# Optimization experiments

Measured on AMD Instinct MI355X. Metric: run time of the kernel, lower is better.

The kernel has to match this reference:

```python
import jax, jax.numpy as jnp
import numpy as np

B, S, D, H, DFF = 2, 4096, 512, 8, 2048
DK = D // H
EPS = 1e-6


def layer_norm(x, alpha, bias):
    # torch: (x - mean) / (std + eps), std unbiased (ddof=1), eps added to std
    mean = jnp.mean(x, axis=-1, keepdims=True)
    std = jnp.std(x, axis=-1, keepdims=True, ddof=1)
    return alpha * (x - mean) / (std + EPS) + bias


def setup_inputs() -> dict:
    key = jax.random.key(0)
    ks = jax.random.split(key, 10)
    s = 0.02
    return {
        "x": jax.random.normal(ks[0], (B, S, D), jnp.float32),
        "mask": jax.random.randint(ks[1], (S, S), 0, 2, jnp.int32),
        "w_q": jax.random.normal(ks[2], (D, D), jnp.float32) * s,
        "w_k": jax.random.normal(ks[3], (D, D), jnp.float32) * s,
        "w_v": jax.random.normal(ks[4], (D, D), jnp.float32) * s,
        "w_o": jax.random.normal(ks[5], (D, D), jnp.float32) * s,
        "w1": jax.random.normal(ks[6], (D, DFF), jnp.float32) * s,
        "b1": jnp.zeros((DFF,), jnp.float32),
        "w2": jax.random.normal(ks[7], (DFF, D), jnp.float32) * s,
        "b2": jnp.zeros((D,), jnp.float32),
        "ln1_a": jnp.ones((D,), jnp.float32),
        "ln1_b": jnp.zeros((D,), jnp.float32),
        "ln2_a": jnp.ones((D,), jnp.float32),
        "ln2_b": jnp.zeros((D,), jnp.float32),
    }


def reference(x, mask, w_q, w_k, w_v, w_o, w1, b1, w2, b2, ln1_a, ln1_b, ln2_a, ln2_b):
    # --- sublayer 0: pre-norm self-attention with residual (dropout=0/eval) ---
    h = layer_norm(x, ln1_a, ln1_b)                       # [B,S,D]
    q = (h @ w_q).reshape(B, S, H, DK)
    k = (h @ w_k).reshape(B, S, H, DK)
    v = (h @ w_v).reshape(B, S, H, DK)
    scores = jnp.einsum("bqhd,bkhd->bhqk", q, k) / jnp.sqrt(jnp.float32(DK))
    scores = jnp.where(mask[None, None, :, :] == 0, jnp.float32(-1e9), scores)
    attn = jax.nn.softmax(scores, axis=-1)                # [B,H,S,S]
    ctx = jnp.einsum("bhqk,bkhd->bqhd", attn, v).reshape(B, S, D)
    x = x + ctx @ w_o
    # --- sublayer 1: pre-norm FFN with residual ---
    h2 = layer_norm(x, ln2_a, ln2_b)
    ff = jax.nn.relu(h2 @ w1 + b1) @ w2 + b2
    return x + ff
```

## Files before the change

### kernel.cpp

```cpp
#include <hip/hip_runtime.h>
#include <hip/hip_bf16.h>
#include <stdint.h>

#define S_LEN 4096
#define DMODEL 512
#define NHEAD 8
#define DHEAD 64
#define NTOK 8192

typedef unsigned short ushort_t;
typedef __attribute__((ext_vector_type(8))) short short8;
typedef __attribute__((ext_vector_type(4))) float f32x4;
typedef unsigned long long u64;
typedef __attribute__((ext_vector_type(2))) unsigned uint2v;

__device__ __forceinline__ float bf2f(ushort_t h) {
    union { unsigned u; float f; } c; c.u = ((unsigned)h) << 16; return c.f;
}
__device__ __forceinline__ ushort_t f2bf(float f) {
    union { float f; unsigned u; } c; c.f = f;
    unsigned u = c.u + 0x7fffu + ((c.u >> 16) & 1u);
    return (ushort_t)(u >> 16);
}
__device__ __forceinline__ void glds16(const ushort_t* g, ushort_t* l) {
    __builtin_amdgcn_global_load_lds(
        (const __attribute__((address_space(1))) unsigned int*)g,
        (__attribute__((address_space(3))) unsigned int*)l, 16, 0, 0);
}

__global__ __launch_bounds__(256) void maskbits_kernel(const int* __restrict__ mask,
        u64* __restrict__ mb) {
    size_t id = (size_t)blockIdx.x * 256 + threadIdx.x;
    int v = mask[id];
    u64 bits = __ballot(v != 0);
    if ((threadIdx.x & 63) == 0) mb[id >> 6] = bits;
}

__global__ __launch_bounds__(256) void wtrans_all(const float* __restrict__ wq,
        const float* __restrict__ wk, const float* __restrict__ wv,
        const float* __restrict__ wo, const float* __restrict__ w1,
        const float* __restrict__ w2,
        ushort_t* wqT, ushort_t* wkT, ushort_t* wvT, ushort_t* woT,
        ushort_t* w1T, ushort_t* w2T) {
    __shared__ __attribute__((aligned(16))) ushort_t t[64][72];
    int z = blockIdx.z;
    const float* src; ushort_t* dst; int R, C;
    switch (z) {
        case 0: src = wq; dst = wqT; R = 512;  C = 512;  break;
        case 1: src = wk; dst = wkT; R = 512;  C = 512;  break;
        case 2: src = wv; dst = wvT; R = 512;  C = 512;  break;
        case 3: src = wo; dst = woT; R = 512;  C = 512;  break;
        case 4: src = w1; dst = w1T; R = 512;  C = 2048; break;
        default: src = w2; dst = w2T; R = 2048; C = 512; break;
    }
    int r0 = blockIdx.x * 64, c0 = blockIdx.y * 64;
    if (r0 >= R || c0 >= C) return;
    int tid = threadIdx.x;
    for (int i = tid; i < 4096; i += 256) {
        int r = i >> 6, c = i & 63;
        t[r][c] = f2bf(src[(size_t)(r0 + r) * C + c0 + c]);
    }
    __syncthreads();
    for (int i = tid; i < 512; i += 256) {
        int c = i >> 3, rb = i & 7;
        short8 vv;
#pragma unroll
        for (int j = 0; j < 8; j++) ((ushort_t*)&vv)[j] = t[rb * 8 + j][c];
        *(short8*)(dst + (size_t)(c0 + c) * R + r0 + rb * 8) = vv;
    }
}

__global__ __launch_bounds__(256) void ln_f32(const float* __restrict__ x,
        const float* __restrict__ ga, const float* __restrict__ be,
        ushort_t* __restrict__ out) {
    int tok = blockIdx.x * 4 + (threadIdx.x >> 6);
    int lane = threadIdx.x & 63;
    const float* xr = x + (size_t)tok * DMODEL + lane * 8;
    f32x4 v0 = *(const f32x4*)xr;
    f32x4 v1 = *(const f32x4*)(xr + 4);
    float f[8];
    float s = 0.f, s2 = 0.f;
#pragma unroll
    for (int i = 0; i < 8; i++) {
        f[i] = (i < 4) ? v0[i] : v1[i - 4];
        s += f[i]; s2 += f[i] * f[i];
    }
#pragma unroll
    for (int off = 1; off < 64; off <<= 1) {
        s += __shfl_xor(s, off);
        s2 += __shfl_xor(s2, off);
    }
    float mean = s * (1.f / DMODEL);
    float var = (s2 - (float)DMODEL * mean * mean) * (1.f / (DMODEL - 1));
    var = fmaxf(var, 0.f);
    float inv = 1.f / (sqrtf(var) + 1e-6f);
    short8 o;
#pragma unroll
    for (int i = 0; i < 8; i++) {
        float val = ga[lane * 8 + i] * (f[i] - mean) * inv + be[lane * 8 + i];
        ((ushort_t*)&o)[i] = f2bf(val);
    }
    *(short8*)(out + (size_t)tok * DMODEL + lane * 8) = o;
}

__global__ __launch_bounds__(256) void vtrans(const ushort_t* __restrict__ V,
        ushort_t* __restrict__ VT) {
    __shared__ __attribute__((aligned(16))) ushort_t t[64][72];
    int s0 = blockIdx.x * 64;
    int bh = blockIdx.y;
    int b = bh >> 3, h = bh & 7;
    int tid = threadIdx.x;
    const ushort_t* src = V + ((size_t)b * S_LEN + s0) * DMODEL + h * DHEAD;
    for (int i = tid; i < 512; i += 256) {
        int r = i >> 3, cb = i & 7;
        *(short8*)&t[r][cb * 8] = *(const short8*)(src + (size_t)r * DMODEL + cb * 8);
    }
    __syncthreads();
    ushort_t* dst = VT + (size_t)bh * DHEAD * S_LEN;
    for (int i = tid; i < 512; i += 256) {
        int d = i >> 3, rb = i & 7;
        short8 vv;
#pragma unroll
        for (int j = 0; j < 8; j++) ((ushort_t*)&vv)[j] = t[rb * 8 + j][d];
        *(short8*)(dst + (size_t)d * S_LEN + s0 + rb * 8) = vv;
    }
}

template <int MW, int NW>
__device__ __forceinline__ void gemm_body(const ushort_t* __restrict__ A,
        const ushort_t* __restrict__ BT, void* __restrict__ C,
        int N, int K, float scale, const float* __restrict__ bias,
        const float* __restrict__ res, int relu, int cf32,
        ushort_t* As, ushort_t* Bs, int m0, int n0, int aoff, int coff) {
    int tid = threadIdx.x;
    int wave = tid >> 6, lane = tid & 63;
    int wm = wave >> 1, wn = wave & 1;
    int lr = lane & 15, lg = lane >> 4;
    int srow = lane >> 2, spos = lane & 3;
    int swz = (spos ^ ((srow >> 1) & 3)) * 8;
    int rdw = (lr >> 1) & 3;
    f32x4 acc[MW][NW];
#pragma unroll
    for (int i = 0; i < MW; i++)
#pragma unroll
        for (int j = 0; j < NW; j++) acc[i][j] = (f32x4){0.f, 0.f, 0.f, 0.f};

    const ushort_t* Ag = A + (size_t)(m0 - aoff) * K;
    const ushort_t* Bg = BT + (size_t)n0 * K;

    for (int k0 = 0; k0 < K; k0 += 32) {
        __syncthreads();
        for (int ia = wave; ia < 2 * MW; ia += 4)
            glds16(Ag + (size_t)(ia * 16 + srow) * K + k0 + swz, As + ia * 16 * 32);
        for (int ib = wave; ib < 2 * NW; ib += 4)
            glds16(Bg + (size_t)(ib * 16 + srow) * K + k0 + swz, Bs + ib * 16 * 32);
        __syncthreads();
        short8 af[MW], bfv[NW];
#pragma unroll
        for (int t = 0; t < MW; t++)
            af[t] = *(const short8*)(As + (wm * 16 * MW + t * 16 + lr) * 32 + (lg ^ rdw) * 8);
#pragma unroll
        for (int t = 0; t < NW; t++)
            bfv[t] = *(const short8*)(Bs + (wn * 16 * NW + t * 16 + lr) * 32 + (lg ^ rdw) * 8);
#pragma unroll
        for (int i = 0; i < MW; i++)
#pragma unroll
            for (int j = 0; j < NW; j++)
                acc[i][j] = __builtin_amdgcn_mfma_f32_16x16x32_bf16(af[i], bfv[j], acc[i][j], 0, 0, 0);
    }
#pragma unroll
    for (int i = 0; i < MW; i++) {
        int row = m0 + wm * 16 * MW + i * 16 + lg * 4;
#pragma unroll
        for (int j = 0; j < NW; j++) {
            int col = n0 + wn * 16 * NW + j * 16 + lr;
            float bb = bias ? bias[col] : 0.f;
#pragma unroll
            for (int r = 0; r < 4; r++) {
                float v = acc[i][j][r] * scale + bb;
                if (relu) v = fmaxf(v, 0.f);
                if (res) v += res[(size_t)(row + r) * N + col];
                size_t cidx = (size_t)(row + r - coff) * N + col;
                if (cf32) ((float*)C)[cidx] = v;
                else      ((ushort_t*)C)[cidx] = f2bf(v);
            }
        }
    }
}

__global__ __launch_bounds__(256) void gemm_bt128(const ushort_t* __restrict__ A,
        const ushort_t* __restrict__ BT, void* __restrict__ C,
        int N, int K, float scale, const float* bias, const float* res, int relu,
        int cf32, int m_base, int aoff, int coff) {
    __shared__ __attribute__((aligned(16))) ushort_t As[128 * 32];
    __shared__ __attribute__((aligned(16))) ushort_t Bs[128 * 32];
    gemm_body<4, 4>(A, BT, C, N, K, scale, bias, res, relu, cf32, As, Bs,
                    m_base + blockIdx.x * 128, blockIdx.y * 128, aoff, coff);
}

__global__ __launch_bounds__(256) void gemm_bt128x64(const ushort_t* __restrict__ A,
        const ushort_t* __restrict__ BT, void* __restrict__ C,
        int N, int K, float scale, const float* bias, const float* res, int relu,
        int cf32, int m_base, int aoff, int coff) {
    __shared__ __attribute__((aligned(16))) ushort_t As[128 * 32];
    __shared__ __attribute__((aligned(16))) ushort_t Bs[64 * 32];
    gemm_body<4, 2>(A, BT, C, N, K, scale, bias, res, relu, cf32, As, Bs,
                    m_base + blockIdx.x * 128, blockIdx.y * 64, aoff, coff);
}

__global__ __launch_bounds__(256) void gemm_qkv(const ushort_t* __restrict__ A,
        const ushort_t* __restrict__ wqT, const ushort_t* __restrict__ wkT,
        const ushort_t* __restrict__ wvT,
        ushort_t* __restrict__ Q, ushort_t* __restrict__ Kb, ushort_t* __restrict__ V) {
    __shared__ __attribute__((aligned(16))) ushort_t As[128 * 32];
    __shared__ __attribute__((aligned(16))) ushort_t Bs[128 * 32];
    int z = blockIdx.z;
    const ushort_t* W = (z == 0) ? wqT : ((z == 1) ? wkT : wvT);
    ushort_t* O = (z == 0) ? Q : ((z == 1) ? Kb : V);
    float sc = (z == 0) ? 0.18033688011112042f : 1.f;
    gemm_body<4, 4>(A, W, O, DMODEL, DMODEL, sc, nullptr, nullptr, 0, 0, As, Bs,
                    blockIdx.x * 128, blockIdx.y * 128, 0, 0);
}

__global__ __launch_bounds__(128, 4) void attn_kernel(const ushort_t* __restrict__ Q,
        const ushort_t* __restrict__ K, const ushort_t* __restrict__ VT,
        const unsigned* __restrict__ mb32, ushort_t* __restrict__ Opart,
        float* __restrict__ lpart) {
    __shared__ __attribute__((aligned(16))) ushort_t Ks[2][32 * 64];
    __shared__ __attribute__((aligned(16))) ushort_t Vs[2][64 * 32];
    int qt = blockIdx.x, h = blockIdx.y, zz = blockIdx.z;
    int b = zz >> 1, half = zz & 1;
    int tid = threadIdx.x;
    int wv = __builtin_amdgcn_readfirstlane(tid >> 6);
    int lane = tid & 63;
    int lr = lane & 15, lg = lane >> 4;
    size_t tokbase = (size_t)b * S_LEN;
    int q0 = qt * 64 + wv * 32;
    int k0 = half * (S_LEN / 2);

    const ushort_t* Qp = Q + (tokbase + q0) * DMODEL + h * DHEAD;
    short8 qf[2][2];
#pragma unroll
    for (int u = 0; u < 2; u++) {
        qf[u][0] = *(const short8*)(Qp + (size_t)(u * 16 + lr) * DMODEL + lg * 8);
        qf[u][1] = *(const short8*)(Qp + (size_t)(u * 16 + lr) * DMODEL + 32 + lg * 8);
    }
    f32x4 o[2][4];
#pragma unroll
    for (int u = 0; u < 2; u++)
#pragma unroll
        for (int td = 0; td < 4; td++) o[u][td] = (f32x4){0.f, 0.f, 0.f, 0.f};
    f32x4 den[2] = {(f32x4){0.f, 0.f, 0.f, 0.f}, (f32x4){0.f, 0.f, 0.f, 0.f}};
    short8 ones8;
#pragma unroll
    for (int j = 0; j < 8; j++) ((ushort_t*)&ones8)[j] = 0x3F80;

    int srow = lane >> 3, spos = lane & 7;
    int srow2 = lane >> 2, spos2 = lane & 3;
    int kst = (spos ^ srow) * 8;
    int vst = (spos2 ^ ((srow2 >> 1) & 3)) * 8;
    int rdk = lr & 7;
    int rdv = (lr >> 1) & 3;

    const ushort_t* kgl = K + (tokbase + k0) * DMODEL + h * DHEAD
                          + (size_t)srow * DMODEL + kst;
    const ushort_t* vgl = VT + (size_t)(b * NHEAD + h) * DHEAD * S_LEN
                          + (size_t)srow2 * S_LEN + k0 + vst;
    const unsigned* mr0 = mb32 + (size_t)(q0 + lr) * 128 + half * 64;
    const unsigned* mr1 = mb32 + (size_t)(q0 + 16 + lr) * 128 + half * 64;

    unsigned w0 = mr0[0], w1 = mr1[0];
    if (wv == 0) {
        glds16(kgl + (size_t)0 * DMODEL, &Ks[0][0 * 64]);
        glds16(kgl + (size_t)8 * DMODEL, &Ks[0][8 * 64]);
        glds16(vgl + (size_t)0 * S_LEN, &Vs[0][0 * 32]);
        glds16(vgl + (size_t)16 * S_LEN, &Vs[0][16 * 32]);
    } else {
        glds16(kgl + (size_t)16 * DMODEL, &Ks[0][16 * 64]);
        glds16(kgl + (size_t)24 * DMODEL, &Ks[0][24 * 64]);
        glds16(vgl + (size_t)32 * S_LEN, &Vs[0][32 * 32]);
        glds16(vgl + (size_t)48 * S_LEN, &Vs[0][48 * 32]);
    }

    const int NIT = (S_LEN / 2) / 32;
#pragma unroll 1
    for (int kt = 0; kt < NIT; kt++) {
        int cur = kt & 1;
        __builtin_amdgcn_s_barrier();
        unsigned nw0 = 0, nw1 = 0;
        if (kt + 1 < NIT) {
            nw0 = mr0[kt + 1];
            nw1 = mr1[kt + 1];
            const ushort_t* kgn = kgl + (size_t)(kt + 1) * 32 * DMODEL;
            const ushort_t* vgn = vgl + (kt + 1) * 32;
            if (wv == 0) {
                glds16(kgn + (size_t)0 * DMODEL, &Ks[cur ^ 1][0 * 64]);
                glds16(kgn + (size_t)8 * DMODEL, &Ks[cur ^ 1][8 * 64]);
                glds16(vgn + (size_t)0 * S_LEN, &Vs[cur ^ 1][0 * 32]);
                glds16(vgn + (size_t)16 * S_LEN, &Vs[cur ^ 1][16 * 32]);
            } else {
                glds16(kgn + (size_t)16 * DMODEL, &Ks[cur ^ 1][16 * 64]);
                glds16(kgn + (size_t)24 * DMODEL, &Ks[cur ^ 1][24 * 64]);
                glds16(vgn + (size_t)32 * S_LEN, &Vs[cur ^ 1][32 * 32]);
                glds16(vgn + (size_t)48 * S_LEN, &Vs[cur ^ 1][48 * 32]);
            }
            __builtin_amdgcn_s_waitcnt(3958);
        } else {
            __builtin_amdgcn_s_waitcnt(3952);
        }
        __builtin_amdgcn_s_barrier();
        const ushort_t* Kb_ = Ks[cur];
        const ushort_t* Vb_ = Vs[cur];
        f32x4 s[2][2];
#pragma unroll
        for (int t = 0; t < 2; t++) {
            const ushort_t* kr = Kb_ + (t * 16 + lr) * 64;
            short8 kf0 = *(const short8*)(kr + ((lg ^ rdk) * 8));
            short8 kf1 = *(const short8*)(kr + (((lg + 4) ^ rdk) * 8));
#pragma unroll
            for (int u = 0; u < 2; u++) {
                f32x4 z = (f32x4){0.f, 0.f, 0.f, 0.f};
                z = __builtin_amdgcn_mfma_f32_16x16x32_bf16(kf0, qf[u][0], z, 0, 0, 0);
                z = __builtin_amdgcn_mfma_f32_16x16x32_bf16(kf1, qf[u][1], z, 0, 0, 0);
                s[t][u] = z;
            }
        }
#pragma unroll
        for (int u = 0; u < 2; u++) {
            unsigned wq = (u ? w1 : w0) >> (lg * 4);
#pragma unroll
            for (int r = 0; r < 4; r++) {
                float p0, p1;
                asm("v_exp_f32 %0, %1\n\ts_nop 0" : "=v"(p0) : "v"(s[0][u][r]));
                asm("v_exp_f32 %0, %1\n\ts_nop 0" : "=v"(p1) : "v"(s[1][u][r]));
                p0 = ((wq >> r) & 1u) ? p0 : 0.f;
                p1 = ((wq >> (16 + r)) & 1u) ? p1 : 0.f;
                s[0][u][r] = p0; s[1][u][r] = p1;
            }
        }
        short8 vf[4];
#pragma unroll
        for (int td = 0; td < 4; td++)
            vf[td] = *(const short8*)(Vb_ + (td * 16 + lr) * 32 + ((lg ^ rdv) * 8));
#pragma unroll
        for (int u = 0; u < 2; u++) {
            unsigned c00, c01, c10, c11;
            asm("v_cvt_pk_bf16_f32 %0, %1, %2" : "=v"(c00) : "v"(s[0][u][0]), "v"(s[0][u][1]));
            asm("v_cvt_pk_bf16_f32 %0, %1, %2" : "=v"(c01) : "v"(s[0][u][2]), "v"(s[0][u][3]));
            asm("v_cvt_pk_bf16_f32 %0, %1, %2" : "=v"(c10) : "v"(s[1][u][0]), "v"(s[1][u][1]));
            asm("v_cvt_pk_bf16_f32 %0, %1, %2" : "=v"(c11) : "v"(s[1][u][2]), "v"(s[1][u][3]));
            auto r0 = __builtin_amdgcn_permlane32_swap(c00, c10, false, false);
            auto r1 = __builtin_amdgcn_permlane32_swap(c01, c11, false, false);
            auto p0 = __builtin_amdgcn_permlane16_swap(r0[0], r0[1], false, false);
            auto p1 = __builtin_amdgcn_permlane16_swap(r1[0], r1[1], false, false);
            union { unsigned u32[4]; short8 s8; } pk;
            pk.u32[0] = p0[0]; pk.u32[1] = p1[0]; pk.u32[2] = p0[1]; pk.u32[3] = p1[1];
            short8 pf = pk.s8;
#pragma unroll
            for (int td = 0; td < 4; td++)
                o[u][td] = __builtin_amdgcn_mfma_f32_16x16x32_bf16(pf, vf[td], o[u][td], 0, 0, 0);
            den[u] = __builtin_amdgcn_mfma_f32_16x16x32_bf16(pf, ones8, den[u], 0, 0, 0);
        }
        w0 = nw0; w1 = nw1;
    }
    float* lp = lpart + (size_t)half * (NHEAD * 2 * S_LEN)
                + (size_t)(b * NHEAD + h) * S_LEN + q0;
    if (lr == 0) {
#pragma unroll
        for (int u = 0; u < 2; u++)
#pragma unroll
            for (int r = 0; r < 4; r++)
                lp[u * 16 + lg * 4 + r] = den[u][r];
    }
    ushort_t* Op = Opart + (size_t)half * NTOK * DMODEL;
#pragma unroll
    for (int u = 0; u < 2; u++) {
        size_t rowb = (tokbase + q0 + u * 16 + lg * 4) * DMODEL + h * DHEAD;
#pragma unroll
        for (int td = 0; td < 4; td++) {
            int cc = td * 16 + lr;
            Op[rowb + 0 * DMODEL + cc] = f2bf(o[u][td][0]);
            Op[rowb + 1 * DMODEL + cc] = f2bf(o[u][td][1]);
            Op[rowb + 2 * DMODEL + cc] = f2bf(o[u][td][2]);
            Op[rowb + 3 * DMODEL + cc] = f2bf(o[u][td][3]);
        }
    }
}

__global__ __launch_bounds__(256) void attn_combine(const ushort_t* __restrict__ Oa,
        const ushort_t* __restrict__ Ob, const float* __restrict__ la,
        const float* __restrict__ lb, ushort_t* __restrict__ ctx) {
    size_t idx = ((size_t)blockIdx.x * 256 + threadIdx.x) * 8;
    size_t tok = idx >> 9;
    int col = (int)(idx & 511);
    int h = col >> 6;
    int b = (int)(tok >> 12);
    int q = (int)(tok & 4095);
    size_t li = (size_t)(b * NHEAD + h) * S_LEN + q;
    float inv = 1.f / (la[li] + lb[li]);
    short8 va = *(const short8*)(Oa + idx);
    short8 vb = *(const short8*)(Ob + idx);
    short8 oo;
#pragma unroll
    for (int j = 0; j < 8; j++)
        ((ushort_t*)&oo)[j] = f2bf((bf2f(((const ushort_t*)&va)[j])
                                  + bf2f(((const ushort_t*)&vb)[j])) * inv);
    *(short8*)(ctx + idx) = oo;
}

extern "C" void kernel_launch(void* const* d_in, const int* in_sizes, int n_in,
                              void* d_out, int out_size, void* d_ws, size_t ws_size,
                              hipStream_t stream) {
    (void)in_sizes; (void)n_in; (void)out_size; (void)ws_size;
    const float* x    = (const float*)d_in[0];
    const int*   mask = (const int*)d_in[1];
    const float* w_q  = (const float*)d_in[2];
    const float* w_k  = (const float*)d_in[3];
    const float* w_v  = (const float*)d_in[4];
    const float* w_o  = (const float*)d_in[5];
    const float* w1   = (const float*)d_in[6];
    const float* b1   = (const float*)d_in[7];
    const float* w2   = (const float*)d_in[8];
    const float* b2   = (const float*)d_in[9];
    const float* l1a  = (const float*)d_in[10];
    const float* l1b  = (const float*)d_in[11];
    const float* l2a  = (const float*)d_in[12];
    const float* l2b  = (const float*)d_in[13];

    char* ws = (char*)d_ws;
    const size_t MB = 1024 * 1024;
    const size_t KB = 1024;
    ushort_t* w1T  = (ushort_t*)(ws + 0);
    ushort_t* w2T  = (ushort_t*)(ws + 2 * MB);
    ushort_t* wqT  = (ushort_t*)(ws + 4 * MB);
    ushort_t* wkT  = (ushort_t*)(ws + 4 * MB + 512 * KB);
    ushort_t* wvT  = (ushort_t*)(ws + 5 * MB);
    ushort_t* woT  = (ushort_t*)(ws + 5 * MB + 512 * KB);
    ushort_t* ff1  = (ushort_t*)(ws + 6 * MB);
    ushort_t* h    = (ushort_t*)(ws + 22 * MB);
    ushort_t* VTb  = h;
    ushort_t* h2   = h;
    ushort_t* Qb   = (ushort_t*)(ws + 30 * MB);
    float*    x2f  = (float*)(ws + 30 * MB);
    ushort_t* Kb   = (ushort_t*)(ws + 38 * MB);
    ushort_t* Vb   = (ushort_t*)(ws + 46 * MB);
    ushort_t* ctx  = Vb;
    ushort_t* Opart = ff1;
    float*    lpart = (float*)wqT;
    u64*      mb   = (u64*)d_out;
    float*    out  = (float*)d_out;

    dim3 blk(256);
    maskbits_kernel<<<dim3(65536), blk, 0, stream>>>(mask, mb);
    wtrans_all<<<dim3(32, 32, 6), blk, 0, stream>>>(w_q, w_k, w_v, w_o, w1, w2,
            wqT, wkT, wvT, woT, w1T, w2T);
    ln_f32<<<dim3(NTOK / 4), blk, 0, stream>>>(x, l1a, l1b, h);
    gemm_qkv<<<dim3(64, 4, 3), blk, 0, stream>>>(h, wqT, wkT, wvT, Qb, Kb, Vb);
    vtrans<<<dim3(64, 16), blk, 0, stream>>>(Vb, VTb);
    attn_kernel<<<dim3(64, 8, 4), dim3(128), 0, stream>>>(Qb, Kb, VTb,
            (const unsigned*)mb, Opart, lpart);
    attn_combine<<<dim3(2048), blk, 0, stream>>>(Opart,
            Opart + (size_t)NTOK * DMODEL, lpart, lpart + NHEAD * 2 * S_LEN, ctx);
    gemm_bt128<<<dim3(64, 4), blk, 0, stream>>>(ctx, woT, x2f, 512, 512, 1.f,
            nullptr, x, 0, 1, 0, 0, 0);
    ln_f32<<<dim3(NTOK / 4), blk, 0, stream>>>(x2f, l2a, l2b, h2);
    gemm_bt128<<<dim3(32, 16), blk, 0, stream>>>(h2, w1T, ff1, 2048, 512, 1.f,
            b1, nullptr, 1, 0, 0, 0, 0);
    gemm_bt128x64<<<dim3(32, 8), blk, 0, stream>>>(ff1, w2T, out, 512, 2048, 1.f,
            b2, x2f, 0, 1, 0, 0, 0);
    gemm_bt128<<<dim3(32, 16), blk, 0, stream>>>(h2, w1T, ff1, 2048, 512, 1.f,
            b1, nullptr, 1, 0, 4096, 0, 4096);
    gemm_bt128x64<<<dim3(32, 8), blk, 0, stream>>>(ff1, w2T, out, 512, 2048, 1.f,
            b2, x2f, 0, 1, 4096, 4096, 0);
}
```

Measured before the change: 464.8 us.

## Pre-transpose mask bits to per-lane ballot masks and shrink GEMM tiles to 64x64

```diff
diff --git a/kernel.cpp b/kernel.cpp
--- a/kernel.cpp
+++ b/kernel.cpp
@@ -34,6 +34,25 @@
     int v = mask[id];
     u64 bits = __ballot(v != 0);
     if ((threadIdx.x & 63) == 0) mb[id >> 6] = bits;
+}
+
+__global__ __launch_bounds__(256) void masktrans_kernel(const u64* __restrict__ mb,
+        u64* __restrict__ mbT) {
+    int wid = (int)(((size_t)blockIdx.x * 256 + threadIdx.x) >> 6);
+    int lane = threadIdx.x & 63;
+    int gq = wid >> 7, kt = wid & 127;
+    int lr = lane & 15, lg = lane >> 4;
+    int row = gq * 16 + lr;
+    u64* outp = mbT + ((size_t)gq * 128 + kt) * 8;
+#pragma unroll
+    for (int t = 0; t < 2; t++)
+#pragma unroll
+        for (int r = 0; r < 4; r++) {
+            int col = kt * 32 + t * 16 + lg * 4 + r;
+            u64 w = mb[(size_t)row * 64 + (col >> 6)];
+            u64 bb = __ballot((unsigned)((w >> (col & 63)) & 1));
+            if (lane == t * 4 + r) outp[t * 4 + r] = bb;
+        }
 }
 
 __global__ __launch_bounds__(256) void wtrans_all(const float* __restrict__ wq,
@@ -188,24 +207,14 @@
     }
 }
 
-__global__ __launch_bounds__(256) void gemm_bt128(const ushort_t* __restrict__ A,
+__global__ __launch_bounds__(256) void gemm_bt64(const ushort_t* __restrict__ A,
         const ushort_t* __restrict__ BT, void* __restrict__ C,
         int N, int K, float scale, const float* bias, const float* res, int relu,
         int cf32, int m_base, int aoff, int coff) {
-    __shared__ __attribute__((aligned(16))) ushort_t As[128 * 32];
-    __shared__ __attribute__((aligned(16))) ushort_t Bs[128 * 32];
-    gemm_body<4, 4>(A, BT, C, N, K, scale, bias, res, relu, cf32, As, Bs,
-                    m_base + blockIdx.x * 128, blockIdx.y * 128, aoff, coff);
-}
-
-__global__ __launch_bounds__(256) void gemm_bt128x64(const ushort_t* __restrict__ A,
-        const ushort_t* __restrict__ BT, void* __restrict__ C,
-        int N, int K, float scale, const float* bias, const float* res, int relu,
-        int cf32, int m_base, int aoff, int coff) {
-    __shared__ __attribute__((aligned(16))) ushort_t As[128 * 32];
+    __shared__ __attribute__((aligned(16))) ushort_t As[64 * 32];
     __shared__ __attribute__((aligned(16))) ushort_t Bs[64 * 32];
-    gemm_body<4, 2>(A, BT, C, N, K, scale, bias, res, relu, cf32, As, Bs,
-                    m_base + blockIdx.x * 128, blockIdx.y * 64, aoff, coff);
+    gemm_body<2, 2>(A, BT, C, N, K, scale, bias, res, relu, cf32, As, Bs,
+                    m_base + blockIdx.x * 64, blockIdx.y * 64, aoff, coff);
 }
 
 __global__ __launch_bounds__(256) void gemm_qkv(const ushort_t* __restrict__ A,
@@ -224,7 +233,7 @@
 
 __global__ __launch_bounds__(128, 4) void attn_kernel(const ushort_t* __restrict__ Q,
         const ushort_t* __restrict__ K, const ushort_t* __restrict__ VT,
-        const unsigned* __restrict__ mb32, ushort_t* __restrict__ Opart,
+        const u64* __restrict__ mbT, ushort_t* __restrict__ Opart,
         float* __restrict__ lpart) {
     __shared__ __attribute__((aligned(16))) ushort_t Ks[2][32 * 64];
     __shared__ __attribute__((aligned(16))) ushort_t Vs[2][64 * 32];
@@ -266,10 +275,9 @@
                           + (size_t)srow * DMODEL + kst;
     const ushort_t* vgl = VT + (size_t)(b * NHEAD + h) * DHEAD * S_LEN
                           + (size_t)srow2 * S_LEN + k0 + vst;
-    const unsigned* mr0 = mb32 + (size_t)(q0 + lr) * 128 + half * 64;
-    const unsigned* mr1 = mb32 + (size_t)(q0 + 16 + lr) * 128 + half * 64;
-
-    unsigned w0 = mr0[0], w1 = mr1[0];
+    const u64* mq0 = mbT + (((size_t)(q0 >> 4)) * 128 + half * 64) * 8;
+    const u64* mq1 = mq0 + 128 * 8;
+
     if (wv == 0) {
         glds16(kgl + (size_t)0 * DMODEL, &Ks[0][0 * 64]);
         glds16(kgl + (size_t)8 * DMODEL, &Ks[0][8 * 64]);
@@ -286,11 +294,10 @@
 #pragma unroll 1
     for (int kt = 0; kt < NIT; kt++) {
         int cur = kt & 1;
+        const u64* m0 = mq0 + (size_t)kt * 8;
+        const u64* m1 = mq1 + (size_t)kt * 8;
         __builtin_amdgcn_s_barrier();
-        unsigned nw0 = 0, nw1 = 0;
         if (kt + 1 < NIT) {
-            nw0 = mr0[kt + 1];
-            nw1 = mr1[kt + 1];
             const ushort_t* kgn = kgl + (size_t)(kt + 1) * 32 * DMODEL;
             const ushort_t* vgn = vgl + (kt + 1) * 32;
             if (wv == 0) {
@@ -304,7 +311,7 @@
                 glds16(vgn + (size_t)32 * S_LEN, &Vs[cur ^ 1][32 * 32]);
                 glds16(vgn + (size_t)48 * S_LEN, &Vs[cur ^ 1][48 * 32]);
             }
-            __builtin_amdgcn_s_waitcnt(3958);
+            __builtin_amdgcn_s_waitcnt(3956);
         } else {
             __builtin_amdgcn_s_waitcnt(3952);
         }
@@ -327,14 +334,14 @@
         }
 #pragma unroll
         for (int u = 0; u < 2; u++) {
-            unsigned wq = (u ? w1 : w0) >> (lg * 4);
+            const u64* mu = u ? m1 : m0;
 #pragma unroll
             for (int r = 0; r < 4; r++) {
                 float p0, p1;
                 asm("v_exp_f32 %0, %1\n\ts_nop 0" : "=v"(p0) : "v"(s[0][u][r]));
                 asm("v_exp_f32 %0, %1\n\ts_nop 0" : "=v"(p1) : "v"(s[1][u][r]));
-                p0 = ((wq >> r) & 1u) ? p0 : 0.f;
-                p1 = ((wq >> (16 + r)) & 1u) ? p1 : 0.f;
+                asm("v_cndmask_b32 %0, 0, %1, %2" : "=v"(p0) : "v"(p0), "s"(mu[r]));
+                asm("v_cndmask_b32 %0, 0, %1, %2" : "=v"(p1) : "v"(p1), "s"(mu[4 + r]));
                 s[0][u][r] = p0; s[1][u][r] = p1;
             }
         }
@@ -361,7 +368,6 @@
                 o[u][td] = __builtin_amdgcn_mfma_f32_16x16x32_bf16(pf, vf[td], o[u][td], 0, 0, 0);
             den[u] = __builtin_amdgcn_mfma_f32_16x16x32_bf16(pf, ones8, den[u], 0, 0, 0);
         }
-        w0 = nw0; w1 = nw1;
     }
     float* lp = lpart + (size_t)half * (NHEAD * 2 * S_LEN)
                 + (size_t)(b * NHEAD + h) * S_LEN + q0;
@@ -448,28 +454,30 @@
     ushort_t* Opart = ff1;
     float*    lpart = (float*)wqT;
     u64*      mb   = (u64*)d_out;
+    u64*      mbT  = (u64*)((char*)d_out + 2 * MB);
     float*    out  = (float*)d_out;
 
     dim3 blk(256);
     maskbits_kernel<<<dim3(65536), blk, 0, stream>>>(mask, mb);
+    masktrans_kernel<<<dim3(8192), blk, 0, stream>>>(mb, mbT);
     wtrans_all<<<dim3(32, 32, 6), blk, 0, stream>>>(w_q, w_k, w_v, w_o, w1, w2,
             wqT, wkT, wvT, woT, w1T, w2T);
     ln_f32<<<dim3(NTOK / 4), blk, 0, stream>>>(x, l1a, l1b, h);
     gemm_qkv<<<dim3(64, 4, 3), blk, 0, stream>>>(h, wqT, wkT, wvT, Qb, Kb, Vb);
     vtrans<<<dim3(64, 16), blk, 0, stream>>>(Vb, VTb);
     attn_kernel<<<dim3(64, 8, 4), dim3(128), 0, stream>>>(Qb, Kb, VTb,
-            (const unsigned*)mb, Opart, lpart);
+            mbT, Opart, lpart);
     attn_combine<<<dim3(2048), blk, 0, stream>>>(Opart,
             Opart + (size_t)NTOK * DMODEL, lpart, lpart + NHEAD * 2 * S_LEN, ctx);
-    gemm_bt128<<<dim3(64, 4), blk, 0, stream>>>(ctx, woT, x2f, 512, 512, 1.f,
+    gemm_bt64<<<dim3(128, 8), blk, 0, stream>>>(ctx, woT, x2f, 512, 512, 1.f,
             nullptr, x, 0, 1, 0, 0, 0);
     ln_f32<<<dim3(NTOK / 4), blk, 0, stream>>>(x2f, l2a, l2b, h2);
-    gemm_bt128<<<dim3(32, 16), blk, 0, stream>>>(h2, w1T, ff1, 2048, 512, 1.f,
+    gemm_bt64<<<dim3(64, 32), blk, 0, stream>>>(h2, w1T, ff1, 2048, 512, 1.f,
             b1, nullptr, 1, 0, 0, 0, 0);
-    gemm_bt128x64<<<dim3(32, 8), blk, 0, stream>>>(ff1, w2T, out, 512, 2048, 1.f,
+    gemm_bt64<<<dim3(64, 8), blk, 0, stream>>>(ff1, w2T, out, 512, 2048, 1.f,
             b2, x2f, 0, 1, 0, 0, 0);
-    gemm_bt128<<<dim3(32, 16), blk, 0, stream>>>(h2, w1T, ff1, 2048, 512, 1.f,
+    gemm_bt64<<<dim3(64, 32), blk, 0, stream>>>(h2, w1T, ff1, 2048, 512, 1.f,
             b1, nullptr, 1, 0, 4096, 0, 4096);
-    gemm_bt128x64<<<dim3(32, 8), blk, 0, stream>>>(ff1, w2T, out, 512, 2048, 1.f,
+    gemm_bt64<<<dim3(64, 8), blk, 0, stream>>>(ff1, w2T, out, 512, 2048, 1.f,
             b2, x2f, 0, 1, 4096, 4096, 0);
 }
```

Result: faster. 411.4 us (-11.5%).
